# Kernel optimization log

Measured on AMD Instinct MI355X. Metric: run time of the kernel, lower is better.

Reference implementation:

```python
import jax, jax.numpy as jnp
import numpy as np

N, E, B, H, L = 100000, 800000, 64, 128, 3
NC = 8  # num_classes
HT = H // 2  # trackster hidden
PD = 2 * H + HT  # pooled feature dim = 320


def layer_norm(h, g, b, eps=1e-5):
    mu = jnp.mean(h, axis=-1, keepdims=True)
    var = jnp.mean((h - mu) ** 2, axis=-1, keepdims=True)
    return (h - mu) / jnp.sqrt(var + eps) * g + b


def setup_inputs() -> dict:
    key = jax.random.key(0)
    ks = jax.random.split(key, 20)

    def xavier(k, shape):
        lim = np.sqrt(6.0 / (shape[-2] + shape[-1])).astype(np.float32)
        return jax.random.uniform(k, shape, jnp.float32, -lim, lim)

    return {
        "x": jax.random.normal(ks[0], (N, 4), jnp.float32),
        "edge_index": jax.random.randint(ks[1], (2, E), 0, N, jnp.int32),
        "batch": jnp.sort(jax.random.randint(ks[2], (N,), 0, B, jnp.int32)),
        "ts": jax.random.normal(ks[3], (B, 3), jnp.float32),
        # node encoder
        "enc_W": xavier(ks[4], (4, H)), "enc_b": jnp.zeros((H,), jnp.float32),
        # SAGEConv layers: lin_l (neighbors, with bias), lin_r (root, no bias)
        "sage_Wl": xavier(ks[5], (L, H, H)), "sage_bl": jnp.zeros((L, H), jnp.float32),
        "sage_Wr": xavier(ks[6], (L, H, H)),
        "ln_g": jnp.ones((L, H), jnp.float32), "ln_b": jnp.zeros((L, H), jnp.float32),
        # trackster encoder
        "ts_W1": xavier(ks[7], (3, HT)), "ts_b1": jnp.zeros((HT,), jnp.float32),
        "ts_lng": jnp.ones((HT,), jnp.float32), "ts_lnb": jnp.zeros((HT,), jnp.float32),
        "ts_W2": xavier(ks[8], (HT, HT)), "ts_b2": jnp.zeros((HT,), jnp.float32),
        # classifier
        "cls_lng": jnp.ones((PD,), jnp.float32), "cls_lnb": jnp.zeros((PD,), jnp.float32),
        "cls_W1": xavier(ks[9], (PD, H)), "cls_b1": jnp.zeros((H,), jnp.float32),
        "cls_W2": xavier(ks[10], (H, NC)), "cls_b2": jnp.zeros((NC,), jnp.float32),
    }


def reference(x, edge_index, batch, ts, enc_W, enc_b, sage_Wl, sage_bl, sage_Wr,
              ln_g, ln_b, ts_W1, ts_b1, ts_lng, ts_lnb, ts_W2, ts_b2,
              cls_lng, cls_lnb, cls_W1, cls_b1, cls_W2, cls_b2):
    src, dst = edge_index[0], edge_index[1]
    h = jax.nn.relu(x @ enc_W + enc_b)  # [N, H]
    # in-degree for mean aggregation (isolated nodes -> aggr 0, like PyG)
    deg = jnp.maximum(jax.ops.segment_sum(jnp.ones((E,), h.dtype), dst, num_segments=N), 1.0)
    for i in range(L):
        agg = jax.ops.segment_sum(h[src], dst, num_segments=N) / deg[:, None]  # mean over in-neighbors
        hn = agg @ sage_Wl[i] + sage_bl[i] + h @ sage_Wr[i]  # SAGEConv
        hn = layer_norm(hn, ln_g[i], ln_b[i])
        h = h + jax.nn.relu(hn)  # dropout is identity in eval
    # dense-pool == segment mean + segment max per graph
    cnt = jnp.maximum(jax.ops.segment_sum(jnp.ones((N,), h.dtype), batch, num_segments=B), 1.0)
    g_mean = jax.ops.segment_sum(h, batch, num_segments=B) / cnt[:, None]  # [B, H]
    g_max = jax.ops.segment_max(h, batch, num_segments=B)  # [B, H]
    # trackster encoder
    t = ts @ ts_W1 + ts_b1
    t = jax.nn.relu(layer_norm(t, ts_lng, ts_lnb))
    t = t @ ts_W2 + ts_b2  # [B, HT]
    feat = jnp.concatenate([g_mean, g_max, t], axis=1)  # [B, 320]
    z = layer_norm(feat, cls_lng, cls_lnb)
    z = jax.nn.relu(z @ cls_W1 + cls_b1)
    return z @ cls_W2 + cls_b2  # [B, NC]
```

## Files before the change

### kernel.cpp

```cpp
#include <hip/hip_runtime.h>
#include <hip/hip_bf16.h>

#define HH 128
#define BUK_SH 9
#define BUK 512
#define CAP 8192

typedef __attribute__((ext_vector_type(8))) short short8;
typedef __attribute__((ext_vector_type(4))) float floatx4;
typedef __attribute__((ext_vector_type(2))) float floatx2;

__device__ __forceinline__ ushort f2bf(float f) {
    uint u = __float_as_uint(f);
    uint r = (u + 0x7FFFu + ((u >> 16) & 1u)) >> 16;
    return (ushort)r;
}
__device__ __forceinline__ float bflo(uint p) { return __uint_as_float(p << 16); }
__device__ __forceinline__ float bfhi(uint p) { return __uint_as_float(p & 0xFFFF0000u); }
__device__ __forceinline__ uint packbf(float a, float b) {
    return (uint)f2bf(a) | ((uint)f2bf(b) << 16);
}
__device__ __forceinline__ float bf2f(ushort u) { return __uint_as_float((uint)u << 16); }
__device__ __forceinline__ uchar f2fp8(float v) {
    return (uchar)(__builtin_amdgcn_cvt_pk_fp8_f32(v, v, 0, false) & 0xFF);
}
__device__ __forceinline__ int permc(int c) {
    return (((c & 31) >> 3) << 5) + ((c >> 5) << 3) + (c & 7);
}


__global__ __launch_bounds__(256) void bin_k(
    const int* __restrict__ src, const int* __restrict__ dst,
    int* __restrict__ gcur, uint* __restrict__ ebuf, int E) {
    __shared__ int hist[256];
    __shared__ int base[256];
    int tid = threadIdx.x;
    hist[tid] = 0;
    __syncthreads();
    int e0 = blockIdx.x * 2048;
    int d[8];
#pragma unroll
    for (int i = 0; i < 8; i++) {
        int e = e0 + i * 256 + tid;
        d[i] = (e < E) ? dst[e] : -1;
        if (d[i] >= 0) atomicAdd(&hist[d[i] >> BUK_SH], 1);
    }
    __syncthreads();
    if (hist[tid] > 0) base[tid] = atomicAdd(&gcur[tid], hist[tid]);
    hist[tid] = 0;
    __syncthreads();
#pragma unroll
    for (int i = 0; i < 8; i++) {
        if (d[i] >= 0) {
            int e = e0 + i * 256 + tid;
            int b = d[i] >> BUK_SH;
            int p = base[b] + atomicAdd(&hist[b], 1);
            if (p < CAP)
                ebuf[(size_t)b * CAP + p] = ((uint)(d[i] & (BUK - 1)) << 17) | (uint)src[e];
        }
    }
}

__global__ __launch_bounds__(256) void build_k(
    const uint* __restrict__ ebuf, const int* __restrict__ gcur,
    int* __restrict__ offs, float* __restrict__ invd,
    int* __restrict__ csr, int N, int nbuk) {
    __shared__ int ncnt[BUK];
    __shared__ int npre[BUK];
    __shared__ int ss[256];
    __shared__ int csrbuf[CAP];
    int b = blockIdx.x, tid = threadIdx.x;

    int bc = (tid < nbuk) ? gcur[tid] : 0;
    if (bc > CAP) bc = CAP;
    ss[tid] = bc;
    __syncthreads();
    for (int o = 1; o < 256; o <<= 1) {
        int tv = (tid >= o) ? ss[tid - o] : 0;
        __syncthreads();
        ss[tid] += tv;
        __syncthreads();
    }
    int cnt = gcur[b]; if (cnt > CAP) cnt = CAP;
    int base = ss[b] - cnt;
    __syncthreads();

    ncnt[tid] = 0; ncnt[tid + 256] = 0;
    __syncthreads();
    const uint* eb = ebuf + (size_t)b * CAP;
    for (int i = tid; i < cnt; i += 256) atomicAdd(&ncnt[eb[i] >> 17], 1);
    __syncthreads();
    int a0 = ncnt[2 * tid], a1 = ncnt[2 * tid + 1];
    int pair = a0 + a1;
    ss[tid] = pair;
    __syncthreads();
    for (int o = 1; o < 256; o <<= 1) {
        int tv = (tid >= o) ? ss[tid - o] : 0;
        __syncthreads();
        ss[tid] += tv;
        __syncthreads();
    }
    int ep = ss[tid] - pair;
    npre[2 * tid] = ep;
    npre[2 * tid + 1] = ep + a0;
    __syncthreads();
#pragma unroll
    for (int q = 0; q < 2; q++) {
        int ln = q * 256 + tid;
        int node = b * BUK + ln;
        if (node < N) {
            offs[node] = base + npre[ln];
            int dg = ncnt[ln];
            invd[node] = 1.0f / (float)(dg > 1 ? dg : 1);
        }
    }
    __syncthreads();
    ncnt[2 * tid] = npre[2 * tid];
    ncnt[2 * tid + 1] = npre[2 * tid + 1];
    __syncthreads();
    for (int i = tid; i < cnt; i += 256) {
        uint pk = eb[i];
        int p = atomicAdd(&ncnt[pk >> 17], 1);
        csrbuf[p] = (int)(pk & 0x1FFFFu);
    }
    __syncthreads();
    for (int i = tid; i < cnt; i += 256) csr[base + i] = csrbuf[i];
    if (b == nbuk - 1 && tid == 0) offs[N] = base + cnt;
}


__global__ __launch_bounds__(256) void prep_w_k(
    const float* __restrict__ Wl, const float* __restrict__ Wr, ushort* __restrict__ Bp) {
    int gid = blockIdx.x * 256 + threadIdx.x;
    int layer = gid >> 15;
    int r = gid & 32767;
    int j = r & 7;
    int lane = (r >> 3) & 63;
    int ct = (r >> 9) & 7;
    int ks = r >> 12;
    int k = ks * 32 + (lane >> 4) * 8 + j;
    int n = ct * 16 + (lane & 15);
    float v = (k < HH) ? Wl[(size_t)layer * HH * HH + k * HH + n]
                       : Wr[(size_t)layer * HH * HH + (k - HH) * HH + n];
    Bp[gid] = f2bf(v);
}


__global__ __launch_bounds__(256) void encoder_k(
    const float* __restrict__ x, const float* __restrict__ W,
    const float* __restrict__ b, uint* __restrict__ hb, uchar* __restrict__ hf8, int N) {
    int n = blockIdx.x * 4 + (threadIdx.x >> 6);
    int j = threadIdx.x & 63;
    if (n >= N) return;
    float4 xv = *(const float4*)(x + (size_t)n * 4);
    float v0 = b[2 * j], v1 = b[2 * j + 1];
    v0 = fmaf(xv.x, W[0 * HH + 2 * j], v0); v1 = fmaf(xv.x, W[0 * HH + 2 * j + 1], v1);
    v0 = fmaf(xv.y, W[1 * HH + 2 * j], v0); v1 = fmaf(xv.y, W[1 * HH + 2 * j + 1], v1);
    v0 = fmaf(xv.z, W[2 * HH + 2 * j], v0); v1 = fmaf(xv.z, W[2 * HH + 2 * j + 1], v1);
    v0 = fmaf(xv.w, W[3 * HH + 2 * j], v0); v1 = fmaf(xv.w, W[3 * HH + 2 * j + 1], v1);
    v0 = fmaxf(v0, 0.0f); v1 = fmaxf(v1, 0.0f);
    hb[(size_t)n * 64 + j] = packbf(v0, v1);
    uint p8 = __builtin_amdgcn_cvt_pk_fp8_f32(v0, v1, 0, false);
    int pos = permc(2 * j);
    ((ushort*)hf8)[(size_t)n * 64 + (pos >> 1)] = (ushort)(p8 & 0xFFFF);
}


__device__ __forceinline__ void acc_u32(float* a, uint u) {
    floatx2 lo = __builtin_amdgcn_cvt_pk_f32_fp8(u, false);
    floatx2 hi = __builtin_amdgcn_cvt_pk_f32_fp8(u, true);
    a[0] += lo.x; a[1] += lo.y; a[2] += hi.x; a[3] += hi.y;
}

__device__ __forceinline__ void gather_agg(
    const uchar* __restrict__ hf8, const int* __restrict__ offs,
    const int* __restrict__ csr, const float* __restrict__ invd,
    int row, int aq, short8* out) {
    const uint4* h8 = (const uint4*)hf8;
    int s = offs[row], e = offs[row + 1];
    float iv = invd[row];
    float ac[4][8];
#pragma unroll
    for (int q = 0; q < 4; q++)
#pragma unroll
        for (int c = 0; c < 8; c++) ac[q][c] = 0.0f;
    int i = s;
    for (; i + 2 <= e; i += 2) {
        int u0 = csr[i], u1 = csr[i + 1];
        uint4 pa0 = h8[(size_t)u0 * 8 + aq * 2];
        uint4 pb0 = h8[(size_t)u0 * 8 + aq * 2 + 1];
        uint4 pa1 = h8[(size_t)u1 * 8 + aq * 2];
        uint4 pb1 = h8[(size_t)u1 * 8 + aq * 2 + 1];
        acc_u32(&ac[0][0], pa0.x); acc_u32(&ac[0][4], pa0.y);
        acc_u32(&ac[1][0], pa0.z); acc_u32(&ac[1][4], pa0.w);
        acc_u32(&ac[2][0], pb0.x); acc_u32(&ac[2][4], pb0.y);
        acc_u32(&ac[3][0], pb0.z); acc_u32(&ac[3][4], pb0.w);
        acc_u32(&ac[0][0], pa1.x); acc_u32(&ac[0][4], pa1.y);
        acc_u32(&ac[1][0], pa1.z); acc_u32(&ac[1][4], pa1.w);
        acc_u32(&ac[2][0], pb1.x); acc_u32(&ac[2][4], pb1.y);
        acc_u32(&ac[3][0], pb1.z); acc_u32(&ac[3][4], pb1.w);
    }
    for (; i < e; i++) {
        int u = csr[i];
        uint4 pa = h8[(size_t)u * 8 + aq * 2];
        uint4 pb = h8[(size_t)u * 8 + aq * 2 + 1];
        acc_u32(&ac[0][0], pa.x); acc_u32(&ac[0][4], pa.y);
        acc_u32(&ac[1][0], pa.z); acc_u32(&ac[1][4], pa.w);
        acc_u32(&ac[2][0], pb.x); acc_u32(&ac[2][4], pb.y);
        acc_u32(&ac[3][0], pb.z); acc_u32(&ac[3][4], pb.w);
    }
#pragma unroll
    for (int q = 0; q < 4; q++) {
        short8 o;
#pragma unroll
        for (int c = 0; c < 8; c++) o[c] = (short)f2bf(ac[q][c] * iv);
        out[q] = o;
    }
}


__global__ __launch_bounds__(256) void sage_mfma_k(
    const ushort* __restrict__ hbin, const uchar* __restrict__ hf8in,
    ushort* __restrict__ hbout, uchar* __restrict__ hf8out,
    const int* __restrict__ offs, const int* __restrict__ csr,
    const float* __restrict__ invd, const ushort* __restrict__ Bp,
    const float* __restrict__ bl, const float* __restrict__ g,
    const float* __restrict__ bln, int N) {
    int wave = threadIdx.x >> 6;
    int lane = threadIdx.x & 63;
    int m0 = blockIdx.x * 128 + wave * 32;
    int am = lane & 15, aq = lane >> 4;

    short8 a_agg[2][4];
#pragma unroll
    for (int rt = 0; rt < 2; rt++) {
        int row = m0 + rt * 16 + am;
        row = row < N ? row : N - 1;
        gather_agg(hf8in, offs, csr, invd, row, aq, a_agg[rt]);
    }

    floatx4 acc[2][8];
#pragma unroll
    for (int rt = 0; rt < 2; rt++)
#pragma unroll
        for (int ct = 0; ct < 8; ct++) acc[rt][ct] = (floatx4)0.0f;

#pragma unroll
    for (int ks = 0; ks < 8; ks++) {
        short8 a[2];
        if (ks < 4) {
            a[0] = a_agg[0][ks];
            a[1] = a_agg[1][ks];
        } else {
            int kc = (ks & 3) * 32 + aq * 8;
#pragma unroll
            for (int rt = 0; rt < 2; rt++) {
                int row = m0 + rt * 16 + am;
                row = row < N ? row : N - 1;
                a[rt] = *(const short8*)(hbin + (size_t)row * HH + kc);
            }
        }
#pragma unroll
        for (int ct = 0; ct < 8; ct++) {
            short8 b = *(const short8*)(Bp + (((size_t)(ks * 8 + ct)) * 64 + lane) * 8);
            acc[0][ct] = __builtin_amdgcn_mfma_f32_16x16x32_bf16(a[0], b, acc[0][ct], 0, 0, 0);
            acc[1][ct] = __builtin_amdgcn_mfma_f32_16x16x32_bf16(a[1], b, acc[1][ct], 0, 0, 0);
        }
    }

    int g4 = lane >> 4, cl = lane & 15;
    float bias[8], gam[8], bet[8];
#pragma unroll
    for (int ct = 0; ct < 8; ct++) {
        bias[ct] = bl[ct * 16 + cl];
        gam[ct] = g[ct * 16 + cl];
        bet[ct] = bln[ct * 16 + cl];
    }
#pragma unroll
    for (int rt = 0; rt < 2; rt++) {
        float sr[4], qr[4];
#pragma unroll
        for (int reg = 0; reg < 4; reg++) {
            float s = 0.0f, q = 0.0f;
#pragma unroll
            for (int ct = 0; ct < 8; ct++) {
                float v = acc[rt][ct][reg] + bias[ct];
                s += v;
                q += v * v;
            }
#pragma unroll
            for (int m = 1; m < 16; m <<= 1) {
                s += __shfl_xor(s, m);
                q += __shfl_xor(q, m);
            }
            sr[reg] = s;
            qr[reg] = q;
        }
#pragma unroll
        for (int reg = 0; reg < 4; reg++) {
            int row = m0 + rt * 16 + g4 * 4 + reg;
            if (row < N) {
                float mean = sr[reg] * (1.0f / 128.0f);
                float var = qr[reg] * (1.0f / 128.0f) - mean * mean;
                float rstd = rsqrtf(fmaxf(var, 0.0f) + 1e-5f);
#pragma unroll
                for (int ct = 0; ct < 8; ct++) {
                    float v = acc[rt][ct][reg] + bias[ct];
                    float r = fmaxf((v - mean) * rstd * gam[ct] + bet[ct], 0.0f);
                    int c = ct * 16 + cl;
                    size_t idx = (size_t)row * HH + c;
                    float nv = bf2f(hbin[idx]) + r;
                    hbout[idx] = f2bf(nv);
                    hf8out[(size_t)row * HH + permc(c)] = f2fp8(nv);
                }
            }
        }
    }
}


__global__ __launch_bounds__(256) void sage_pool_k(
    const ushort* __restrict__ hbin, const uchar* __restrict__ hf8in,
    const int* __restrict__ offs, const int* __restrict__ csr,
    const float* __restrict__ invd, const ushort* __restrict__ Bp,
    const float* __restrict__ bl, const float* __restrict__ g,
    const float* __restrict__ bln, const int* __restrict__ batch,
    float* __restrict__ psum, int* __restrict__ pmax, int* __restrict__ pcnt, int N) {
    __shared__ float wsum[4][128];
    __shared__ float wmax[4][128];
    __shared__ int wcnt[4];
    int tid = threadIdx.x;
    int wave = tid >> 6;
    int lane = tid & 63;
    int blk0 = blockIdx.x * 128;
    int m0 = blk0 + wave * 32;
    int am = lane & 15, aq = lane >> 4;

    short8 a_agg[2][4];
#pragma unroll
    for (int rt = 0; rt < 2; rt++) {
        int row = m0 + rt * 16 + am;
        row = row < N ? row : N - 1;
        gather_agg(hf8in, offs, csr, invd, row, aq, a_agg[rt]);
    }

    floatx4 acc[2][8];
#pragma unroll
    for (int rt = 0; rt < 2; rt++)
#pragma unroll
        for (int ct = 0; ct < 8; ct++) acc[rt][ct] = (floatx4)0.0f;

#pragma unroll
    for (int ks = 0; ks < 8; ks++) {
        short8 a[2];
        if (ks < 4) {
            a[0] = a_agg[0][ks];
            a[1] = a_agg[1][ks];
        } else {
            int kc = (ks & 3) * 32 + aq * 8;
#pragma unroll
            for (int rt = 0; rt < 2; rt++) {
                int row = m0 + rt * 16 + am;
                row = row < N ? row : N - 1;
                a[rt] = *(const short8*)(hbin + (size_t)row * HH + kc);
            }
        }
#pragma unroll
        for (int ct = 0; ct < 8; ct++) {
            short8 b = *(const short8*)(Bp + (((size_t)(ks * 8 + ct)) * 64 + lane) * 8);
            acc[0][ct] = __builtin_amdgcn_mfma_f32_16x16x32_bf16(a[0], b, acc[0][ct], 0, 0, 0);
            acc[1][ct] = __builtin_amdgcn_mfma_f32_16x16x32_bf16(a[1], b, acc[1][ct], 0, 0, 0);
        }
    }

    int g4 = lane >> 4, cl = lane & 15;
    float bias[8], gam[8], bet[8];
#pragma unroll
    for (int ct = 0; ct < 8; ct++) {
        bias[ct] = bl[ct * 16 + cl];
        gam[ct] = g[ct * 16 + cl];
        bet[ct] = bln[ct * 16 + cl];
    }
#pragma unroll
    for (int rt = 0; rt < 2; rt++) {
        float sr[4], qr[4];
#pragma unroll
        for (int reg = 0; reg < 4; reg++) {
            float s = 0.0f, q = 0.0f;
#pragma unroll
            for (int ct = 0; ct < 8; ct++) {
                float v = acc[rt][ct][reg] + bias[ct];
                s += v;
                q += v * v;
            }
#pragma unroll
            for (int m = 1; m < 16; m <<= 1) {
                s += __shfl_xor(s, m);
                q += __shfl_xor(q, m);
            }
            sr[reg] = s;
            qr[reg] = q;
        }
#pragma unroll
        for (int reg = 0; reg < 4; reg++) {
            int row = m0 + rt * 16 + g4 * 4 + reg;
            float mean = sr[reg] * (1.0f / 128.0f);
            float var = qr[reg] * (1.0f / 128.0f) - mean * mean;
            float rstd = rsqrtf(fmaxf(var, 0.0f) + 1e-5f);
            if (row < N) {
#pragma unroll
                for (int ct = 0; ct < 8; ct++) {
                    float v = acc[rt][ct][reg] + bias[ct];
                    float r = fmaxf((v - mean) * rstd * gam[ct] + bet[ct], 0.0f);
                    acc[rt][ct][reg] = bf2f(hbin[(size_t)row * HH + ct * 16 + cl]) + r;
                }
            } else {
#pragma unroll
                for (int ct = 0; ct < 8; ct++) acc[rt][ct][reg] = 0.0f;
            }
        }
    }

    bool fast = (blk0 + 127 < N) && (batch[blk0] == batch[blk0 + 127]);
    if (fast) {
        int b0 = batch[blk0];
#pragma unroll
        for (int ct = 0; ct < 8; ct++) {
            float s = 0.0f, m = 0.0f;
#pragma unroll
            for (int rt = 0; rt < 2; rt++)
#pragma unroll
                for (int reg = 0; reg < 4; reg++) {
                    float v = acc[rt][ct][reg];
                    s += v;
                    m = fmaxf(m, v);
                }
            s += __shfl_xor(s, 16); m = fmaxf(m, __shfl_xor(m, 16));
            s += __shfl_xor(s, 32); m = fmaxf(m, __shfl_xor(m, 32));
            if (g4 == 0) {
                wsum[wave][ct * 16 + cl] = s;
                wmax[wave][ct * 16 + cl] = m;
            }
        }
        __syncthreads();
        if (tid < 128) {
            float s = (wsum[0][tid] + wsum[1][tid]) + (wsum[2][tid] + wsum[3][tid]);
            float m = fmaxf(fmaxf(wmax[0][tid], wmax[1][tid]),
                            fmaxf(wmax[2][tid], wmax[3][tid]));
            atomicAdd(&psum[b0 * HH + tid], s);
            atomicMax(&pmax[b0 * HH + tid], __float_as_int(m));
        }
        if (tid == 0) atomicAdd(&pcnt[b0], 128);
    } else {
        int nlast = (blk0 + 127 < N - 1) ? blk0 + 127 : N - 1;
        int bfirst = batch[blk0];
        int blast = batch[nlast];
        int brow[2][4];
#pragma unroll
        for (int rt = 0; rt < 2; rt++)
#pragma unroll
            for (int reg = 0; reg < 4; reg++) {
                int row = m0 + rt * 16 + g4 * 4 + reg;
                brow[rt][reg] = (row < N) ? batch[row] : -1;
            }
        for (int b = bfirst; b <= blast; b++) {
            int c = 0;
#pragma unroll
            for (int rt = 0; rt < 2; rt++)
#pragma unroll
                for (int reg = 0; reg < 4; reg++) c += (brow[rt][reg] == b) ? 1 : 0;
            c += __shfl_xor(c, 16);
            c += __shfl_xor(c, 32);
#pragma unroll
            for (int ct = 0; ct < 8; ct++) {
                float s = 0.0f, m = 0.0f;
#pragma unroll
                for (int rt = 0; rt < 2; rt++)
#pragma unroll
                    for (int reg = 0; reg < 4; reg++) {
                        if (brow[rt][reg] == b) {
                            float v = acc[rt][ct][reg];
                            s += v;
                            m = fmaxf(m, v);
                        }
                    }
                s += __shfl_xor(s, 16); m = fmaxf(m, __shfl_xor(m, 16));
                s += __shfl_xor(s, 32); m = fmaxf(m, __shfl_xor(m, 32));
                if (g4 == 0) {
                    wsum[wave][ct * 16 + cl] = s;
                    wmax[wave][ct * 16 + cl] = m;
                }
            }
            if (lane == 0) wcnt[wave] = c;
            __syncthreads();
            if (tid < 128) {
                float s = (wsum[0][tid] + wsum[1][tid]) + (wsum[2][tid] + wsum[3][tid]);
                float m = fmaxf(fmaxf(wmax[0][tid], wmax[1][tid]),
                                fmaxf(wmax[2][tid], wmax[3][tid]));
                atomicAdd(&psum[b * HH + tid], s);
                atomicMax(&pmax[b * HH + tid], __float_as_int(m));
            }
            if (tid == 0)
                atomicAdd(&pcnt[b], wcnt[0] + wcnt[1] + wcnt[2] + wcnt[3]);
            __syncthreads();
        }
    }
}


__global__ __launch_bounds__(128) void head_k(
    const float* __restrict__ psum, const float* __restrict__ pmax,
    const int* __restrict__ pcnt, const float* __restrict__ ts,
    const float* __restrict__ tsW1, const float* __restrict__ tsb1,
    const float* __restrict__ tslng, const float* __restrict__ tslnb,
    const float* __restrict__ tsW2, const float* __restrict__ tsb2,
    const float* __restrict__ clng, const float* __restrict__ clnb,
    const float* __restrict__ cW1, const float* __restrict__ cb1,
    const float* __restrict__ cW2, const float* __restrict__ cb2,
    float* __restrict__ out) {
    int b = blockIdx.x;
    int t = threadIdx.x;
    __shared__ float feat[320];
    __shared__ float tn[64];
    __shared__ float zz[128];
    __shared__ float ps[2], pq[2];

    if (t < 64) {
        float v = tsb1[t];
#pragma unroll
        for (int k = 0; k < 3; k++) v = fmaf(ts[b * 3 + k], tsW1[k * 64 + t], v);
        float s = v, q = v * v;
#pragma unroll
        for (int m = 1; m < 64; m <<= 1) {
            s += __shfl_xor(s, m);
            q += __shfl_xor(q, m);
        }
        float mean = s * (1.0f / 64.0f);
        float var = q * (1.0f / 64.0f) - mean * mean;
        float rstd = rsqrtf(fmaxf(var, 0.0f) + 1e-5f);
        tn[t] = fmaxf((v - mean) * rstd * tslng[t] + tslnb[t], 0.0f);
    }
    __syncthreads();
    if (t < 64) {
        float v = tsb2[t];
        for (int k = 0; k < 64; k++) v = fmaf(tn[k], tsW2[k * 64 + t], v);
        feat[256 + t] = v;
    }
    float cntf = (float)(pcnt[b] > 1 ? pcnt[b] : 1);
    feat[t] = psum[b * HH + t] / cntf;
    feat[128 + t] = pmax[b * HH + t];
    __syncthreads();

    float s = 0.0f, q = 0.0f;
    for (int i = t; i < 320; i += 128) {
        float v = feat[i];
        s += v;
        q += v * v;
    }
#pragma unroll
    for (int m = 1; m < 64; m <<= 1) {
        s += __shfl_xor(s, m);
        q += __shfl_xor(q, m);
    }
    if ((t & 63) == 0) { ps[t >> 6] = s; pq[t >> 6] = q; }
    __syncthreads();
    float S = ps[0] + ps[1], Q = pq[0] + pq[1];
    float mean = S * (1.0f / 320.0f);
    float var = Q * (1.0f / 320.0f) - mean * mean;
    float rstd = rsqrtf(fmaxf(var, 0.0f) + 1e-5f);
    for (int i = t; i < 320; i += 128)
        feat[i] = (feat[i] - mean) * rstd * clng[i] + clnb[i];
    __syncthreads();

    {
        float v = cb1[t];
        for (int k = 0; k < 320; k++) v = fmaf(feat[k], cW1[k * HH + t], v);
        zz[t] = fmaxf(v, 0.0f);
    }
    __syncthreads();
    if (t < 8) {
        float v = cb2[t];
        for (int k = 0; k < 128; k++) v = fmaf(zz[k], cW2[k * 8 + t], v);
        out[b * 8 + t] = v;
    }
}


extern "C" void kernel_launch(void* const* d_in, const int* in_sizes, int n_in,
                              void* d_out, int out_size, void* d_ws, size_t ws_size,
                              hipStream_t stream) {
    const int N = in_sizes[0] / 4;
    const int E = in_sizes[1] / 2;
    const int B = in_sizes[3] / 3;
    const int nbuk = (N + BUK - 1) >> BUK_SH;

    const float* x    = (const float*)d_in[0];
    const int*   ei   = (const int*)d_in[1];
    const int*   srcv = ei;
    const int*   dstv = ei + E;
    const int*   batch = (const int*)d_in[2];
    const float* ts   = (const float*)d_in[3];
    const float* encW = (const float*)d_in[4];
    const float* encb = (const float*)d_in[5];
    const float* sageWl = (const float*)d_in[6];
    const float* sagebl = (const float*)d_in[7];
    const float* sageWr = (const float*)d_in[8];
    const float* lng  = (const float*)d_in[9];
    const float* lnb  = (const float*)d_in[10];
    const float* tsW1 = (const float*)d_in[11];
    const float* tsb1 = (const float*)d_in[12];
    const float* tslng = (const float*)d_in[13];
    const float* tslnb = (const float*)d_in[14];
    const float* tsW2 = (const float*)d_in[15];
    const float* tsb2 = (const float*)d_in[16];
    const float* clng = (const float*)d_in[17];
    const float* clnb = (const float*)d_in[18];
    const float* cW1  = (const float*)d_in[19];
    const float* cb1  = (const float*)d_in[20];
    const float* cW2  = (const float*)d_in[21];
    const float* cb2  = (const float*)d_in[22];
    float* out = (float*)d_out;

    char* w = (char*)d_ws;
    size_t off = 0;
    auto take = [&](size_t bytes) -> void* {
        void* p = w + off;
        off = (off + bytes + 255) & ~(size_t)255;
        return p;
    };
    uint*  hb0  = (uint*)take((size_t)N * HH * 2);
    uint*  hb1  = (uint*)take((size_t)N * HH * 2);
    uchar* hf80 = (uchar*)take((size_t)N * HH);
    uchar* hf81 = (uchar*)take((size_t)N * HH);
    ushort* Bp  = (ushort*)take((size_t)3 * HH * 2 * HH * 2);
    int*   csr  = (int*)take((size_t)E * 4);
    int*   offs = (int*)take((size_t)(N + 1) * 4);
    float* invd = (float*)take((size_t)N * 4);
    uint*  ebuf = (uint*)take((size_t)nbuk * CAP * 4);
    size_t z0 = off;
    int*   gcur = (int*)take(256 * 4);
    float* psum = (float*)take((size_t)B * HH * 4);
    int*   pmax = (int*)take((size_t)B * HH * 4);
    int*   pcnt = (int*)take((size_t)B * 4);
    size_t z1 = off;

    hipMemsetAsync(w + z0, 0, z1 - z0, stream);

    bin_k<<<(E + 2047) / 2048, 256, 0, stream>>>(srcv, dstv, gcur, ebuf, E);
    build_k<<<nbuk, 256, 0, stream>>>(ebuf, gcur, offs, invd, csr, N, nbuk);

    prep_w_k<<<384, 256, 0, stream>>>(sageWl, sageWr, Bp);
    encoder_k<<<(N + 3) / 4, 256, 0, stream>>>(x, encW, encb, hb0, hf80, N);

    int nblk = (N + 127) / 128;
    sage_mfma_k<<<nblk, 256, 0, stream>>>(
        (const ushort*)hb0, hf80, (ushort*)hb1, hf81, offs, csr, invd, Bp,
        sagebl, lng, lnb, N);
    sage_mfma_k<<<nblk, 256, 0, stream>>>(
        (const ushort*)hb1, hf81, (ushort*)hb0, hf80, offs, csr, invd,
        Bp + (size_t)32768,
        sagebl + (size_t)HH, lng + (size_t)HH, lnb + (size_t)HH, N);
    sage_pool_k<<<nblk, 256, 0, stream>>>(
        (const ushort*)hb0, hf80, offs, csr, invd, Bp + (size_t)2 * 32768,
        sagebl + (size_t)2 * HH, lng + (size_t)2 * HH, lnb + (size_t)2 * HH,
        batch, psum, pmax, pcnt, N);

    head_k<<<B, 128, 0, stream>>>(psum, (const float*)pmax, pcnt, ts,
                                  tsW1, tsb1, tslng, tslnb, tsW2, tsb2,
                                  clng, clnb, cW1, cb1, cW2, cb2, out);
}
```

Before: 344.7 us.

## Split neighbor aggregation into separate kernel writing bf16 agg buffer

Moves the fp8 neighbor gather-and-mean out of the MFMA SAGE kernels into a dedicated aggregate kernel that uses 8 threads per node with 4-way edge unrolling and writes a bf16 aggregate buffer. The MFMA kernels then load the aggregate from memory like a dense operand. The aim is to decouple the latency-bound irregular gather from the MFMA-heavy kernel so each can get better occupancy and memory parallelism. In exchange it adds three kernel launches and an extra N×128 bf16 write and read per layer.

```diff
diff --git a/kernel.cpp b/kernel.cpp
--- a/kernel.cpp
+++ b/kernel.cpp
@@ -166,79 +166,63 @@
 }
 
 
-__device__ __forceinline__ void acc_u32(float* a, uint u) {
-    floatx2 lo = __builtin_amdgcn_cvt_pk_f32_fp8(u, false);
-    floatx2 hi = __builtin_amdgcn_cvt_pk_f32_fp8(u, true);
-    a[0] += lo.x; a[1] += lo.y; a[2] += hi.x; a[3] += hi.y;
-}
-
-__device__ __forceinline__ void gather_agg(
+__device__ __forceinline__ void acc16(float* a, uint4 p) {
+    floatx2 v;
+    v = __builtin_amdgcn_cvt_pk_f32_fp8(p.x, false); a[0] += v.x;  a[1] += v.y;
+    v = __builtin_amdgcn_cvt_pk_f32_fp8(p.x, true);  a[2] += v.x;  a[3] += v.y;
+    v = __builtin_amdgcn_cvt_pk_f32_fp8(p.y, false); a[4] += v.x;  a[5] += v.y;
+    v = __builtin_amdgcn_cvt_pk_f32_fp8(p.y, true);  a[6] += v.x;  a[7] += v.y;
+    v = __builtin_amdgcn_cvt_pk_f32_fp8(p.z, false); a[8] += v.x;  a[9] += v.y;
+    v = __builtin_amdgcn_cvt_pk_f32_fp8(p.z, true);  a[10] += v.x; a[11] += v.y;
+    v = __builtin_amdgcn_cvt_pk_f32_fp8(p.w, false); a[12] += v.x; a[13] += v.y;
+    v = __builtin_amdgcn_cvt_pk_f32_fp8(p.w, true);  a[14] += v.x; a[15] += v.y;
+}
+
+__global__ __launch_bounds__(256) void aggregate_k(
     const uchar* __restrict__ hf8, const int* __restrict__ offs,
     const int* __restrict__ csr, const float* __restrict__ invd,
-    int row, int aq, short8* out) {
+    uint* __restrict__ aggb, int N) {
+    int n = blockIdx.x * 32 + (threadIdx.x >> 3);
+    int j = threadIdx.x & 7;
+    if (n >= N) return;
     const uint4* h8 = (const uint4*)hf8;
-    int s = offs[row], e = offs[row + 1];
-    float iv = invd[row];
-    float ac[4][8];
-#pragma unroll
-    for (int q = 0; q < 4; q++)
-#pragma unroll
-        for (int c = 0; c < 8; c++) ac[q][c] = 0.0f;
+    int s = offs[n], e = offs[n + 1];
+    float ac[16];
+#pragma unroll
+    for (int k = 0; k < 16; k++) ac[k] = 0.0f;
     int i = s;
-    for (; i + 2 <= e; i += 2) {
-        int u0 = csr[i], u1 = csr[i + 1];
-        uint4 pa0 = h8[(size_t)u0 * 8 + aq * 2];
-        uint4 pb0 = h8[(size_t)u0 * 8 + aq * 2 + 1];
-        uint4 pa1 = h8[(size_t)u1 * 8 + aq * 2];
-        uint4 pb1 = h8[(size_t)u1 * 8 + aq * 2 + 1];
-        acc_u32(&ac[0][0], pa0.x); acc_u32(&ac[0][4], pa0.y);
-        acc_u32(&ac[1][0], pa0.z); acc_u32(&ac[1][4], pa0.w);
-        acc_u32(&ac[2][0], pb0.x); acc_u32(&ac[2][4], pb0.y);
-        acc_u32(&ac[3][0], pb0.z); acc_u32(&ac[3][4], pb0.w);
-        acc_u32(&ac[0][0], pa1.x); acc_u32(&ac[0][4], pa1.y);
-        acc_u32(&ac[1][0], pa1.z); acc_u32(&ac[1][4], pa1.w);
-        acc_u32(&ac[2][0], pb1.x); acc_u32(&ac[2][4], pb1.y);
-        acc_u32(&ac[3][0], pb1.z); acc_u32(&ac[3][4], pb1.w);
+    for (; i + 4 <= e; i += 4) {
+        int u0 = csr[i], u1 = csr[i + 1], u2 = csr[i + 2], u3 = csr[i + 3];
+        uint4 p0 = h8[(size_t)u0 * 8 + j];
+        uint4 p1 = h8[(size_t)u1 * 8 + j];
+        uint4 p2 = h8[(size_t)u2 * 8 + j];
+        uint4 p3 = h8[(size_t)u3 * 8 + j];
+        acc16(ac, p0); acc16(ac, p1); acc16(ac, p2); acc16(ac, p3);
     }
     for (; i < e; i++) {
-        int u = csr[i];
-        uint4 pa = h8[(size_t)u * 8 + aq * 2];
-        uint4 pb = h8[(size_t)u * 8 + aq * 2 + 1];
-        acc_u32(&ac[0][0], pa.x); acc_u32(&ac[0][4], pa.y);
-        acc_u32(&ac[1][0], pa.z); acc_u32(&ac[1][4], pa.w);
-        acc_u32(&ac[2][0], pb.x); acc_u32(&ac[2][4], pb.y);
-        acc_u32(&ac[3][0], pb.z); acc_u32(&ac[3][4], pb.w);
-    }
-#pragma unroll
-    for (int q = 0; q < 4; q++) {
-        short8 o;
-#pragma unroll
-        for (int c = 0; c < 8; c++) o[c] = (short)f2bf(ac[q][c] * iv);
-        out[q] = o;
-    }
+        uint4 p = h8[(size_t)csr[i] * 8 + j];
+        acc16(ac, p);
+    }
+    float iv = invd[n];
+    uint o[8];
+#pragma unroll
+    for (int k = 0; k < 8; k++) o[k] = packbf(ac[2 * k] * iv, ac[2 * k + 1] * iv);
+    uint4* outp = (uint4*)(aggb + (size_t)n * 64 + j * 8);
+    outp[0] = make_uint4(o[0], o[1], o[2], o[3]);
+    outp[1] = make_uint4(o[4], o[5], o[6], o[7]);
 }
 
 
 __global__ __launch_bounds__(256) void sage_mfma_k(
-    const ushort* __restrict__ hbin, const uchar* __restrict__ hf8in,
+    const ushort* __restrict__ hbin, const uint* __restrict__ aggb,
     ushort* __restrict__ hbout, uchar* __restrict__ hf8out,
-    const int* __restrict__ offs, const int* __restrict__ csr,
-    const float* __restrict__ invd, const ushort* __restrict__ Bp,
-    const float* __restrict__ bl, const float* __restrict__ g,
-    const float* __restrict__ bln, int N) {
+    const ushort* __restrict__ Bp, const float* __restrict__ bl,
+    const float* __restrict__ g, const float* __restrict__ bln, int N) {
     int wave = threadIdx.x >> 6;
     int lane = threadIdx.x & 63;
     int m0 = blockIdx.x * 128 + wave * 32;
     int am = lane & 15, aq = lane >> 4;
 
-    short8 a_agg[2][4];
-#pragma unroll
-    for (int rt = 0; rt < 2; rt++) {
-        int row = m0 + rt * 16 + am;
-        row = row < N ? row : N - 1;
-        gather_agg(hf8in, offs, csr, invd, row, aq, a_agg[rt]);
-    }
-
     floatx4 acc[2][8];
 #pragma unroll
     for (int rt = 0; rt < 2; rt++)
@@ -248,16 +232,14 @@
 #pragma unroll
     for (int ks = 0; ks < 8; ks++) {
         short8 a[2];
-        if (ks < 4) {
-            a[0] = a_agg[0][ks];
-            a[1] = a_agg[1][ks];
-        } else {
-            int kc = (ks & 3) * 32 + aq * 8;
-#pragma unroll
-            for (int rt = 0; rt < 2; rt++) {
-                int row = m0 + rt * 16 + am;
-                row = row < N ? row : N - 1;
-                a[rt] = *(const short8*)(hbin + (size_t)row * HH + kc);
+#pragma unroll
+        for (int rt = 0; rt < 2; rt++) {
+            int row = m0 + rt * 16 + am;
+            row = row < N ? row : N - 1;
+            if (ks < 4) {
+                a[rt] = *(const short8*)(aggb + (size_t)row * 64 + aq * 16 + ks * 4);
+            } else {
+                a[rt] = *(const short8*)(hbin + (size_t)row * HH + (ks & 3) * 32 + aq * 8);
             }
         }
 #pragma unroll
@@ -320,11 +302,10 @@
 
 
 __global__ __launch_bounds__(256) void sage_pool_k(
-    const ushort* __restrict__ hbin, const uchar* __restrict__ hf8in,
-    const int* __restrict__ offs, const int* __restrict__ csr,
-    const float* __restrict__ invd, const ushort* __restrict__ Bp,
-    const float* __restrict__ bl, const float* __restrict__ g,
-    const float* __restrict__ bln, const int* __restrict__ batch,
+    const ushort* __restrict__ hbin, const uint* __restrict__ aggb,
+    const ushort* __restrict__ Bp, const float* __restrict__ bl,
+    const float* __restrict__ g, const float* __restrict__ bln,
+    const int* __restrict__ batch,
     float* __restrict__ psum, int* __restrict__ pmax, int* __restrict__ pcnt, int N) {
     __shared__ float wsum[4][128];
     __shared__ float wmax[4][128];
@@ -336,14 +317,6 @@
     int m0 = blk0 + wave * 32;
     int am = lane & 15, aq = lane >> 4;
 
-    short8 a_agg[2][4];
-#pragma unroll
-    for (int rt = 0; rt < 2; rt++) {
-        int row = m0 + rt * 16 + am;
-        row = row < N ? row : N - 1;
-        gather_agg(hf8in, offs, csr, invd, row, aq, a_agg[rt]);
-    }
-
     floatx4 acc[2][8];
 #pragma unroll
     for (int rt = 0; rt < 2; rt++)
@@ -353,16 +326,14 @@
 #pragma unroll
     for (int ks = 0; ks < 8; ks++) {
         short8 a[2];
-        if (ks < 4) {
-            a[0] = a_agg[0][ks];
-            a[1] = a_agg[1][ks];
-        } else {
-            int kc = (ks & 3) * 32 + aq * 8;
-#pragma unroll
-            for (int rt = 0; rt < 2; rt++) {
-                int row = m0 + rt * 16 + am;
-                row = row < N ? row : N - 1;
-                a[rt] = *(const short8*)(hbin + (size_t)row * HH + kc);
+#pragma unroll
+        for (int rt = 0; rt < 2; rt++) {
+            int row = m0 + rt * 16 + am;
+            row = row < N ? row : N - 1;
+            if (ks < 4) {
+                a[rt] = *(const short8*)(aggb + (size_t)row * 64 + aq * 16 + ks * 4);
+            } else {
+                a[rt] = *(const short8*)(hbin + (size_t)row * HH + (ks & 3) * 32 + aq * 8);
             }
         }
 #pragma unroll
@@ -632,6 +603,7 @@
     uint*  hb1  = (uint*)take((size_t)N * HH * 2);
     uchar* hf80 = (uchar*)take((size_t)N * HH);
     uchar* hf81 = (uchar*)take((size_t)N * HH);
+    uint*  aggb = (uint*)take((size_t)N * HH * 2);
     ushort* Bp  = (ushort*)take((size_t)3 * HH * 2 * HH * 2);
     int*   csr  = (int*)take((size_t)E * 4);
     int*   offs = (int*)take((size_t)(N + 1) * 4);
@@ -653,15 +625,18 @@
     encoder_k<<<(N + 3) / 4, 256, 0, stream>>>(x, encW, encb, hb0, hf80, N);
 
     int nblk = (N + 127) / 128;
+    int ablk = (N + 31) / 32;
+    aggregate_k<<<ablk, 256, 0, stream>>>(hf80, offs, csr, invd, aggb, N);
     sage_mfma_k<<<nblk, 256, 0, stream>>>(
-        (const ushort*)hb0, hf80, (ushort*)hb1, hf81, offs, csr, invd, Bp,
+        (const ushort*)hb0, aggb, (ushort*)hb1, hf81, Bp,
         sagebl, lng, lnb, N);
+    aggregate_k<<<ablk, 256, 0, stream>>>(hf81, offs, csr, invd, aggb, N);
     sage_mfma_k<<<nblk, 256, 0, stream>>>(
-        (const ushort*)hb1, hf81, (ushort*)hb0, hf80, offs, csr, invd,
-        Bp + (size_t)32768,
+        (const ushort*)hb1, aggb, (ushort*)hb0, hf80, Bp + (size_t)32768,
         sagebl + (size_t)HH, lng + (size_t)HH, lnb + (size_t)HH, N);
+    aggregate_k<<<ablk, 256, 0, stream>>>(hf80, offs, csr, invd, aggb, N);
     sage_pool_k<<<nblk, 256, 0, stream>>>(
-        (const ushort*)hb0, hf80, offs, csr, invd, Bp + (size_t)2 * 32768,
+        (const ushort*)hb0, aggb, Bp + (size_t)2 * 32768,
         sagebl + (size_t)2 * HH, lng + (size_t)2 * HH, lnb + (size_t)2 * HH,
         batch, psum, pmax, pcnt, N);
 
```

Result: no change. 347.6 us (+0.8%).
